# Performance work log

Hardware: AMD Instinct MI355X
Metric: run time of the kernel (lower is better)

## Reference

```python
import jax, jax.numpy as jnp
import numpy as np

D_MODEL = 2048
NUM_HEADS = 16
HEAD_DIM = D_MODEL // NUM_HEADS
SCALE = 1.0 / np.sqrt(HEAD_DIM).astype(np.float32)
NEG_INF = -1e9


def setup_inputs() -> dict:
    key = jax.random.key(0)
    ks = jax.random.split(key, 10)
    B, S = 2, 2048
    x = jax.random.normal(ks[0], (B, S, D_MODEL), dtype=jnp.float32)
    # causal lower-triangular mask, broadcastable over (B, H)
    causal_mask = jnp.tril(jnp.ones((S, S), dtype=jnp.int32))[None, None]
    init = 1.0 / np.sqrt(D_MODEL)
    def lin(kw, kb):
        W = jax.random.uniform(kw, (D_MODEL, D_MODEL), jnp.float32, -init, init)
        b = jax.random.uniform(kb, (D_MODEL,), jnp.float32, -init, init)
        return W, b
    Wq, bq = lin(ks[1], ks[2])
    Wk, bk = lin(ks[3], ks[4])
    Wv, bv = lin(ks[5], ks[6])
    Wo, bo = lin(ks[7], ks[8])
    return {"x": x, "causal_mask": causal_mask,
            "Wq": Wq, "bq": bq, "Wk": Wk, "bk": bk,
            "Wv": Wv, "bv": bv, "Wo": Wo, "bo": bo}


def reference(x, causal_mask, Wq, bq, Wk, bk, Wv, bv, Wo, bo):
    B, S, _ = x.shape
    def proj(W, b):
        # torch Linear: x @ W.T + b -> (B, H, S, Dh)
        y = jnp.einsum('bsd,ed->bse', x, W) + b
        return y.reshape(B, S, NUM_HEADS, HEAD_DIM).transpose(0, 2, 1, 3)
    q = proj(Wq, bq)
    k = proj(Wk, bk)
    v = proj(Wv, bv)
    # apply_rope is a no-op stub in the source; q, k unchanged.
    scores = jnp.einsum('bhqd,bhkd->bhqk', q, k) * SCALE
    scores = jnp.where(causal_mask == 0, NEG_INF, scores)
    attn = jax.nn.softmax(scores, axis=-1)
    out = jnp.einsum('bhqk,bhkd->bhqd', attn, v)
    out = out.transpose(0, 2, 1, 3).reshape(B, S, D_MODEL)
    return jnp.einsum('bsd,ed->bse', out, Wo) + bo
```

## Files before the change

kernel.cpp:

```cpp
#include <hip/hip_runtime.h>
#include <hip/hip_bf16.h>
#include <stdint.h>
#include <stddef.h>

typedef __bf16 bf16_t;
typedef __bf16 bf16x4_t __attribute__((ext_vector_type(4)));
typedef __bf16 bf16x8_t __attribute__((ext_vector_type(8)));
typedef float f32x4 __attribute__((ext_vector_type(4)));

#define D_MODEL 2048
#define NHEADS 16
#define HDIM 128
#define SEQ 2048
#define BATCH 2
#define MTOT (BATCH * SEQ)
#define SCALE_F 0.08838834764831845f
#define LOG2E 1.4426950408889634f
#define QSCALE (SCALE_F * LOG2E)
#define KT 64
#define NEGI -3.0e38f
#define MINIT -1.0e30f
#define DEFER_THR 8.0f

#define AS1 __attribute__((address_space(1)))
#define AS3 __attribute__((address_space(3)))

__device__ __forceinline__ void load_lds16(const bf16_t* g, bf16_t* l) {
  __builtin_amdgcn_global_load_lds((AS1 void*)(g), (AS3 void*)(l), 16, 0, 0);
}

__global__ void cast_kernel(const float* __restrict__ src, bf16_t* __restrict__ dst, int n4) {
  int i = blockIdx.x * blockDim.x + threadIdx.x;
  if (i < n4) {
    float4 v = ((const float4*)src)[i];
    bf16x4_t o;
    o.x = (bf16_t)v.x; o.y = (bf16_t)v.y; o.z = (bf16_t)v.z; o.w = (bf16_t)v.w;
    ((bf16x4_t*)dst)[i] = o;
  }
}

__global__ void cast4_kernel(const float* __restrict__ s0, const float* __restrict__ s1,
                             const float* __restrict__ s2, const float* __restrict__ s3,
                             bf16_t* __restrict__ dst, int n4) {
  int i = blockIdx.x * blockDim.x + threadIdx.x;
  int y = blockIdx.y;
  if (i < n4) {
    const float* src = (y == 0) ? s0 : (y == 1) ? s1 : (y == 2) ? s2 : s3;
    float4 v = ((const float4*)src)[i];
    bf16x4_t o;
    o.x = (bf16_t)v.x; o.y = (bf16_t)v.y; o.z = (bf16_t)v.z; o.w = (bf16_t)v.w;
    ((bf16x4_t*)(dst + (size_t)y * D_MODEL * D_MODEL / 4 * 4))[i] = o;
  }
}

__global__ __launch_bounds__(256) void gemm_fused(
    const bf16_t* __restrict__ A, const bf16_t* __restrict__ Bm, int mode,
    const float* __restrict__ bias0, const float* __restrict__ bias1,
    const float* __restrict__ bias2,
    bf16_t* __restrict__ Qo, bf16_t* __restrict__ Ko, bf16_t* __restrict__ Vto,
    float* __restrict__ Out) {
  const int K = 2048;
  __shared__ __align__(16) bf16_t lA[128 * 64];
  __shared__ __align__(16) bf16_t lB[128 * 64];
  const int m0 = blockIdx.x * 128;
  const int n0 = blockIdx.y * 128;
  const int t = threadIdx.x;
  const int w = t >> 6, lane = t & 63;
  const int wm = w & 1, wn = w >> 1;
  const int la = lane & 15, lb = lane >> 4;

  f32x4 acc[4][4];
  f32x4 zero = {0.f, 0.f, 0.f, 0.f};
#pragma unroll
  for (int i = 0; i < 4; i++)
#pragma unroll
    for (int j = 0; j < 4; j++) acc[i][j] = zero;

  const int row0 = t >> 3, cc = t & 7;
  const int ccs = cc ^ (row0 & 7);
  const bf16_t* gA = A + (size_t)(m0 + row0) * K + ccs * 8;
  const bf16_t* gB = Bm + (size_t)(n0 + row0) * K + ccs * 8;
  bf16_t* sA = lA + t * 8;
  bf16_t* sB = lB + t * 8;

  for (int k0 = 0; k0 < K; k0 += 64) {
    __syncthreads();
#pragma unroll
    for (int i = 0; i < 4; i++)
      load_lds16(gA + k0 + (size_t)(32 * i) * K, sA + 2048 * i);
#pragma unroll
    for (int i = 0; i < 4; i++)
      load_lds16(gB + k0 + (size_t)(32 * i) * K, sB + 2048 * i);
    __syncthreads();
#pragma unroll
    for (int ks = 0; ks < 2; ks++) {
      bf16x8_t af[4], bfr[4];
#pragma unroll
      for (int mt = 0; mt < 4; mt++) {
        int row = wm * 64 + mt * 16 + la;
        af[mt] = *(const bf16x8_t*)(lA + row * 64 + (((ks * 4 + lb) ^ (la & 7)) * 8));
      }
#pragma unroll
      for (int nt = 0; nt < 4; nt++) {
        int row = wn * 64 + nt * 16 + la;
        bfr[nt] = *(const bf16x8_t*)(lB + row * 64 + (((ks * 4 + lb) ^ (la & 7)) * 8));
      }
#pragma unroll
      for (int mt = 0; mt < 4; mt++)
#pragma unroll
        for (int nt = 0; nt < 4; nt++)
          acc[mt][nt] = __builtin_amdgcn_mfma_f32_16x16x32_bf16(af[mt], bfr[nt], acc[mt][nt], 0, 0, 0);
    }
  }

  if (mode == 0) {
#pragma unroll
    for (int mt = 0; mt < 4; mt++) {
#pragma unroll
      for (int nt = 0; nt < 4; nt++) {
        int m = m0 + wm * 64 + mt * 16 + lb * 4;
        int n = n0 + wn * 64 + nt * 16 + la;
        int b = m >> 11, s = m & 2047;
        int which = n >> 11, hd = n & 2047;
        int h = hd >> 7, d = hd & 127;
        float bv = (which == 0 ? bias0 : which == 1 ? bias1 : bias2)[hd];
        f32x4 v = acc[mt][nt];
        if (which == 2) {
          bf16_t* dst = Vto + ((size_t)(b * NHEADS + h) * HDIM + d) * SEQ + s;
          bf16x4_t pk;
          pk.x = (bf16_t)(v.x + bv); pk.y = (bf16_t)(v.y + bv);
          pk.z = (bf16_t)(v.z + bv); pk.w = (bf16_t)(v.w + bv);
          *(bf16x4_t*)dst = pk;
        } else {
          float sc = (which == 0) ? QSCALE : 1.0f;
          bf16_t* dst = (which == 0 ? Qo : Ko) + ((size_t)(b * NHEADS + h) * SEQ + s) * HDIM + d;
          dst[0]        = (bf16_t)((v.x + bv) * sc);
          dst[HDIM]     = (bf16_t)((v.y + bv) * sc);
          dst[2 * HDIM] = (bf16_t)((v.z + bv) * sc);
          dst[3 * HDIM] = (bf16_t)((v.w + bv) * sc);
        }
      }
    }
  } else {
#pragma unroll
    for (int mt = 0; mt < 4; mt++) {
#pragma unroll
      for (int nt = 0; nt < 4; nt++) {
        int m = m0 + wm * 64 + mt * 16 + lb * 4;
        int n = n0 + wn * 64 + nt * 16 + la;
        float bv = bias0[n];
        f32x4 v = acc[mt][nt];
        float* dst = Out + (size_t)m * D_MODEL + n;
        dst[0]           = v.x + bv;
        dst[D_MODEL]     = v.y + bv;
        dst[2 * D_MODEL] = v.z + bv;
        dst[3 * D_MODEL] = v.w + bv;
      }
    }
  }
}

__global__ __launch_bounds__(256, 2) void flash_attn(
    const bf16_t* __restrict__ Q, const bf16_t* __restrict__ Kg,
    const bf16_t* __restrict__ Vt, bf16_t* __restrict__ O,
    bf16_t* __restrict__ PO, float* __restrict__ ML) {
  __shared__ __align__(16) bf16_t lK[2][KT * 128];
  __shared__ __align__(16) bf16_t lV[128 * KT];
  __shared__ __align__(16) bf16_t lP[128 * 72];
  const int g = blockIdx.x;
  const int bh = g & 31, idx = g >> 5;
  const int t = threadIdx.x;
  const int w = t >> 6, lane = t & 63;
  const int la = lane & 15, lb = lane >> 4;
  const int qloc = w * 32 + la;

  const bf16_t* Qb = Q + (size_t)bh * SEQ * HDIM;
  const bf16_t* Kb = Kg + (size_t)bh * SEQ * HDIM;
  const bf16_t* Vb = Vt + (size_t)bh * HDIM * SEQ;
  const int b = bh >> 4, h = bh & 15;

  int nph, qts[2], k0s[2], k1s[2], slots[2];
  bool parts[2];
  if (idx < 8) {
    nph = 1; qts[0] = 8 + idx; k0s[0] = 0; k1s[0] = 17;
    parts[0] = true; slots[0] = (idx * 32 + bh) * 2;
  } else {
    int qtA = idx - 8;
    nph = 2;
    qts[0] = qtA; k0s[0] = 0; k1s[0] = 2 * qtA + 2; parts[0] = false; slots[0] = 0;
    qts[1] = 15 - qtA; k0s[1] = 17; k1s[1] = 32 - 2 * qtA;
    parts[1] = true; slots[1] = ((7 - qtA) * 32 + bh) * 2 + 1;
  }

  const int krow = t >> 4, kcc = t & 15;
  const int kccx = kcc ^ krow;
  const int vrow = t >> 3, vjc = t & 7;
  const int vccx = vjc ^ (vrow & 7);

  for (int ph = 0; ph < nph; ph++) {
    const int qt = qts[ph], kt0 = k0s[ph], kt1 = k1s[ph];
    const int q0 = qt * 128;

    bf16x8_t qf[2][4];
#pragma unroll
    for (int mt = 0; mt < 2; mt++)
#pragma unroll
      for (int ks = 0; ks < 4; ks++)
        qf[mt][ks] = *(const bf16x8_t*)(Qb + (size_t)(q0 + qloc + mt * 16) * HDIM + ks * 32 + lb * 8);

    f32x4 oacc[2][8];
    float mr[2] = {MINIT, MINIT}, lr[2] = {0.f, 0.f};
    f32x4 zero = {0.f, 0.f, 0.f, 0.f};
#pragma unroll
    for (int mt = 0; mt < 2; mt++)
#pragma unroll
      for (int dt = 0; dt < 8; dt++) oacc[mt][dt] = zero;

    {
      const int j0 = kt0 * KT;
#pragma unroll
      for (int i = 0; i < 4; i++)
        load_lds16(Kb + (size_t)(j0 + krow + 16 * i) * HDIM + kccx * 8,
                   lK[kt0 & 1] + (t + 256 * i) * 8);
    }

    for (int kt = kt0; kt < kt1; kt++) {
      const int j0 = kt * KT;
      const int cur = kt & 1;
      const bool pre = (kt + 1 < kt1);

      __syncthreads();

#pragma unroll
      for (int i = 0; i < 4; i++)
        load_lds16(Vb + (size_t)(vrow + 32 * i) * SEQ + j0 + vccx * 8,
                   lV + (t + 256 * i) * 8);
      if (pre) {
        const int jn = (kt + 1) * KT;
#pragma unroll
        for (int i = 0; i < 4; i++)
          load_lds16(Kb + (size_t)(jn + krow + 16 * i) * HDIM + kccx * 8,
                     lK[cur ^ 1] + (t + 256 * i) * 8);
      }

      f32x4 st[4][2];
#pragma unroll
      for (int nt = 0; nt < 4; nt++)
#pragma unroll
        for (int mt = 0; mt < 2; mt++) st[nt][mt] = zero;
#pragma unroll
      for (int ks = 0; ks < 4; ks++) {
#pragma unroll
        for (int nt = 0; nt < 4; nt++) {
          int j = nt * 16 + la;
          int ck = (ks * 4 + lb) ^ la;
          bf16x8_t kf = *(const bf16x8_t*)(lK[cur] + j * 128 + ck * 8);
#pragma unroll
          for (int mt = 0; mt < 2; mt++)
            st[nt][mt] = __builtin_amdgcn_mfma_f32_16x16x32_bf16(kf, qf[mt][ks], st[nt][mt], 0, 0, 0);
        }
      }

      const bool dm = (j0 + KT > q0);
#pragma unroll
      for (int mt = 0; mt < 2; mt++) {
        int qg = q0 + qloc + mt * 16;
        if (dm) {
#pragma unroll
          for (int nt = 0; nt < 4; nt++)
#pragma unroll
            for (int r = 0; r < 4; r++)
              if (j0 + nt * 16 + lb * 4 + r > qg) st[nt][mt][r] = NEGI;
        }
        float tm = NEGI;
#pragma unroll
        for (int nt = 0; nt < 4; nt++)
#pragma unroll
          for (int r = 0; r < 4; r++) tm = fmaxf(tm, st[nt][mt][r]);
        tm = fmaxf(tm, __shfl_xor(tm, 16));
        tm = fmaxf(tm, __shfl_xor(tm, 32));
        if (!__all(tm - mr[mt] <= DEFER_THR)) {
          float mnew = fmaxf(mr[mt], tm);
          float alpha = exp2f(mr[mt] - mnew);
          lr[mt] *= alpha;
#pragma unroll
          for (int dt = 0; dt < 8; dt++) oacc[mt][dt] *= alpha;
          mr[mt] = mnew;
        }
        float s = 0.f;
#pragma unroll
        for (int nt = 0; nt < 4; nt++) {
          f32x4 p;
#pragma unroll
          for (int r = 0; r < 4; r++) {
            p[r] = exp2f(st[nt][mt][r] - mr[mt]);
            s += p[r];
          }
          bf16x4_t pk;
          pk.x = (bf16_t)p[0]; pk.y = (bf16_t)p[1]; pk.z = (bf16_t)p[2]; pk.w = (bf16_t)p[3];
          *(bf16x4_t*)(lP + (qloc + mt * 16) * 72 + nt * 16 + lb * 4) = pk;
        }
        s += __shfl_xor(s, 16);
        s += __shfl_xor(s, 32);
        lr[mt] += s;
      }

      if (pre) {
        asm volatile("s_waitcnt vmcnt(4)" ::: "memory");
      } else {
        asm volatile("s_waitcnt vmcnt(0)" ::: "memory");
      }
      __builtin_amdgcn_s_barrier();

      bf16x8_t pf[2][2];
#pragma unroll
      for (int mt = 0; mt < 2; mt++)
#pragma unroll
        for (int ksv = 0; ksv < 2; ksv++)
          pf[mt][ksv] = *(const bf16x8_t*)(lP + (w * 32 + mt * 16 + la) * 72 + ksv * 32 + lb * 8);
#pragma unroll
      for (int dt = 0; dt < 8; dt++) {
        int d = dt * 16 + la;
#pragma unroll
        for (int ksv = 0; ksv < 2; ksv++) {
          int jc = (ksv * 4 + lb) ^ (d & 7);
          bf16x8_t vf = *(const bf16x8_t*)(lV + d * 64 + jc * 8);
#pragma unroll
          for (int mt = 0; mt < 2; mt++)
            oacc[mt][dt] = __builtin_amdgcn_mfma_f32_16x16x32_bf16(vf, pf[mt][ksv], oacc[mt][dt], 0, 0, 0);
        }
      }
    }

    if (!parts[ph]) {
#pragma unroll
      for (int mt = 0; mt < 2; mt++) {
        float inv = 1.0f / lr[mt];
        int q = q0 + qloc + mt * 16;
        bf16_t* dst = O + ((size_t)b * SEQ + q) * D_MODEL + h * HDIM + lb * 4;
#pragma unroll
        for (int dt = 0; dt < 8; dt++) {
          f32x4 v = oacc[mt][dt];
          bf16x4_t pk;
          pk.x = (bf16_t)(v[0] * inv); pk.y = (bf16_t)(v[1] * inv);
          pk.z = (bf16_t)(v[2] * inv); pk.w = (bf16_t)(v[3] * inv);
          *(bf16x4_t*)(dst + dt * 16) = pk;
        }
      }
    } else {
      const int slot = slots[ph];
      bf16_t* pob = PO + (size_t)slot * 128 * 128;
#pragma unroll
      for (int mt = 0; mt < 2; mt++) {
        int q = qloc + mt * 16;
        bf16_t* dst = pob + (size_t)q * 128 + lb * 4;
#pragma unroll
        for (int dt = 0; dt < 8; dt++) {
          f32x4 v = oacc[mt][dt];
          bf16x4_t pk;
          pk.x = (bf16_t)v[0]; pk.y = (bf16_t)v[1];
          pk.z = (bf16_t)v[2]; pk.w = (bf16_t)v[3];
          *(bf16x4_t*)(dst + dt * 16) = pk;
        }
        if (lb == 0) {
          float2 ml = make_float2(mr[mt], lr[mt]);
          *(float2*)(ML + ((size_t)slot * 128 + q) * 2) = ml;
        }
      }
    }
  }
}

__global__ void merge_kernel(const bf16_t* __restrict__ PO, const float* __restrict__ ML,
                             bf16_t* __restrict__ O) {
  const int qti = blockIdx.x >> 5, bh = blockIdx.x & 31;
  const int qt = 8 + qti;
  const int t = threadIdx.x;
  const int q = t >> 1, dh = (t & 1) * 64;
  const size_t s1 = ((size_t)(qti * 32 + bh)) * 2;
  const float* ml1 = ML + (s1 * 128 + q) * 2;
  const float* ml2 = ML + ((s1 + 1) * 128 + q) * 2;
  float m1 = ml1[0], l1 = ml1[1], m2 = ml2[0], l2 = ml2[1];
  float m = fmaxf(m1, m2);
  float w1 = exp2f(m1 - m), w2 = exp2f(m2 - m);
  float inv = 1.0f / (w1 * l1 + w2 * l2);
  w1 *= inv; w2 *= inv;
  const bf16_t* p1 = PO + (s1 * 128 + q) * 128 + dh;
  const bf16_t* p2 = PO + ((s1 + 1) * 128 + q) * 128 + dh;
  const int b = bh >> 4, h = bh & 15;
  bf16_t* dst = O + ((size_t)b * SEQ + qt * 128 + q) * D_MODEL + h * HDIM + dh;
#pragma unroll
  for (int i = 0; i < 8; i++) {
    bf16x8_t a = ((const bf16x8_t*)p1)[i];
    bf16x8_t c = ((const bf16x8_t*)p2)[i];
    bf16x8_t o;
#pragma unroll
    for (int e = 0; e < 8; e++)
      o[e] = (bf16_t)(w1 * (float)a[e] + w2 * (float)c[e]);
    ((bf16x8_t*)dst)[i] = o;
  }
}

extern "C" void kernel_launch(void* const* d_in, const int* in_sizes, int n_in,
                              void* d_out, int out_size, void* d_ws, size_t ws_size,
                              hipStream_t stream) {
  (void)in_sizes; (void)n_in; (void)out_size; (void)ws_size;
  const float* x  = (const float*)d_in[0];
  const float* Wq = (const float*)d_in[2];
  const float* bq = (const float*)d_in[3];
  const float* Wk = (const float*)d_in[4];
  const float* bk = (const float*)d_in[5];
  const float* Wv = (const float*)d_in[6];
  const float* bv = (const float*)d_in[7];
  const float* Wo = (const float*)d_in[8];
  const float* bo = (const float*)d_in[9];
  float* out = (float*)d_out;

  const size_t NBF = (size_t)MTOT * D_MODEL * sizeof(bf16_t);
  const size_t WBF = (size_t)D_MODEL * D_MODEL * sizeof(bf16_t);
  char* p = (char*)d_ws;
  bf16_t* xb   = (bf16_t*)p; p += NBF;
  bf16_t* Wcat = (bf16_t*)p; p += 4 * WBF;
  bf16_t* Qb   = (bf16_t*)p; p += NBF;
  bf16_t* Kb   = (bf16_t*)p; p += NBF;
  bf16_t* Vtb  = (bf16_t*)p; p += NBF;
  bf16_t* Wob  = Wcat + (size_t)3 * D_MODEL * D_MODEL;
  bf16_t* Ob   = xb;
  bf16_t* PO = Wcat;
  float*  ML = (float*)(Wcat + (size_t)512 * 128 * 128);

  const int WN4 = D_MODEL * D_MODEL / 4;
  const int XN4 = MTOT * D_MODEL / 4;
  cast_kernel<<<XN4 / 256, 256, 0, stream>>>(x, xb, XN4);
  cast4_kernel<<<dim3(WN4 / 256, 4), 256, 0, stream>>>(Wq, Wk, Wv, Wo, Wcat, WN4);

  gemm_fused<<<dim3(MTOT / 128, 6144 / 128), 256, 0, stream>>>(
      xb, Wcat, 0, bq, bk, bv, Qb, Kb, Vtb, nullptr);

  flash_attn<<<dim3(512), 256, 0, stream>>>(Qb, Kb, Vtb, Ob, PO, ML);
  merge_kernel<<<dim3(256), 256, 0, stream>>>(PO, ML, Ob);

  gemm_fused<<<dim3(MTOT / 128, D_MODEL / 128), 256, 0, stream>>>(
      Ob, Wob, 1, bo, nullptr, nullptr, nullptr, nullptr, nullptr, out);
}
```

Measured before the change: 375.2 us.

## Enlarge flash-attention query tile to 256 rows with double-buffered K/V staging

The attention kernel now runs 512 threads per block over 256-query tiles, which halves the grid and doubles the reuse of each K/V tile staged in shared memory. V is now double-buffered alongside K, and the next K/V tile is prefetched together. The mid-iteration vmcnt wait and barrier before the PV step are removed. The causal work-split schedule and the merge kernel are rescaled to match. In exchange, shared memory per block grows, occupancy may drop, and the grid of 256 blocks may leave some CUs underused.

```diff
diff --git a/kernel.cpp b/kernel.cpp
--- a/kernel.cpp
+++ b/kernel.cpp
@@ -160,13 +160,13 @@
   }
 }
 
-__global__ __launch_bounds__(256, 2) void flash_attn(
+__global__ __launch_bounds__(512, 2) void flash_attn(
     const bf16_t* __restrict__ Q, const bf16_t* __restrict__ Kg,
     const bf16_t* __restrict__ Vt, bf16_t* __restrict__ O,
     bf16_t* __restrict__ PO, float* __restrict__ ML) {
   __shared__ __align__(16) bf16_t lK[2][KT * 128];
-  __shared__ __align__(16) bf16_t lV[128 * KT];
-  __shared__ __align__(16) bf16_t lP[128 * 72];
+  __shared__ __align__(16) bf16_t lV[2][128 * KT];
+  __shared__ __align__(16) bf16_t lP[256 * 72];
   const int g = blockIdx.x;
   const int bh = g & 31, idx = g >> 5;
   const int t = threadIdx.x;
@@ -181,25 +181,36 @@
 
   int nph, qts[2], k0s[2], k1s[2], slots[2];
   bool parts[2];
-  if (idx < 8) {
-    nph = 1; qts[0] = 8 + idx; k0s[0] = 0; k1s[0] = 17;
+  if (idx < 4) {
+    nph = 1; qts[0] = 4 + idx; k0s[0] = 0; k1s[0] = 18;
     parts[0] = true; slots[0] = (idx * 32 + bh) * 2;
   } else {
-    int qtA = idx - 8;
+    int qtA = idx - 4;
     nph = 2;
-    qts[0] = qtA; k0s[0] = 0; k1s[0] = 2 * qtA + 2; parts[0] = false; slots[0] = 0;
-    qts[1] = 15 - qtA; k0s[1] = 17; k1s[1] = 32 - 2 * qtA;
-    parts[1] = true; slots[1] = ((7 - qtA) * 32 + bh) * 2 + 1;
+    qts[0] = qtA; k0s[0] = 0; k1s[0] = 4 * qtA + 4; parts[0] = false; slots[0] = 0;
+    qts[1] = 7 - qtA; k0s[1] = 18; k1s[1] = 32 - 4 * qtA;
+    parts[1] = true; slots[1] = ((3 - qtA) * 32 + bh) * 2 + 1;
   }
 
   const int krow = t >> 4, kcc = t & 15;
-  const int kccx = kcc ^ krow;
+  const int kccx = kcc ^ (krow & 15);
   const int vrow = t >> 3, vjc = t & 7;
   const int vccx = vjc ^ (vrow & 7);
 
+  auto stageKV = [&](int buf, int j0) {
+#pragma unroll
+    for (int i = 0; i < 2; i++)
+      load_lds16(Kb + (size_t)(j0 + krow + 32 * i) * HDIM + kccx * 8,
+                 lK[buf] + (t + 512 * i) * 8);
+#pragma unroll
+    for (int i = 0; i < 2; i++)
+      load_lds16(Vb + (size_t)(vrow + 64 * i) * SEQ + j0 + vccx * 8,
+                 lV[buf] + (t + 512 * i) * 8);
+  };
+
   for (int ph = 0; ph < nph; ph++) {
     const int qt = qts[ph], kt0 = k0s[ph], kt1 = k1s[ph];
-    const int q0 = qt * 128;
+    const int q0 = qt * 256;
 
     bf16x8_t qf[2][4];
 #pragma unroll
@@ -216,32 +227,15 @@
 #pragma unroll
       for (int dt = 0; dt < 8; dt++) oacc[mt][dt] = zero;
 
-    {
-      const int j0 = kt0 * KT;
-#pragma unroll
-      for (int i = 0; i < 4; i++)
-        load_lds16(Kb + (size_t)(j0 + krow + 16 * i) * HDIM + kccx * 8,
-                   lK[kt0 & 1] + (t + 256 * i) * 8);
-    }
+    __syncthreads();
+    stageKV(kt0 & 1, kt0 * KT);
 
     for (int kt = kt0; kt < kt1; kt++) {
       const int j0 = kt * KT;
       const int cur = kt & 1;
-      const bool pre = (kt + 1 < kt1);
 
       __syncthreads();
-
-#pragma unroll
-      for (int i = 0; i < 4; i++)
-        load_lds16(Vb + (size_t)(vrow + 32 * i) * SEQ + j0 + vccx * 8,
-                   lV + (t + 256 * i) * 8);
-      if (pre) {
-        const int jn = (kt + 1) * KT;
-#pragma unroll
-        for (int i = 0; i < 4; i++)
-          load_lds16(Kb + (size_t)(jn + krow + 16 * i) * HDIM + kccx * 8,
-                     lK[cur ^ 1] + (t + 256 * i) * 8);
-      }
+      if (kt + 1 < kt1) stageKV(cur ^ 1, (kt + 1) * KT);
 
       f32x4 st[4][2];
 #pragma unroll
@@ -305,26 +299,19 @@
         lr[mt] += s;
       }
 
-      if (pre) {
-        asm volatile("s_waitcnt vmcnt(4)" ::: "memory");
-      } else {
-        asm volatile("s_waitcnt vmcnt(0)" ::: "memory");
-      }
-      __builtin_amdgcn_s_barrier();
-
       bf16x8_t pf[2][2];
 #pragma unroll
       for (int mt = 0; mt < 2; mt++)
 #pragma unroll
         for (int ksv = 0; ksv < 2; ksv++)
-          pf[mt][ksv] = *(const bf16x8_t*)(lP + (w * 32 + mt * 16 + la) * 72 + ksv * 32 + lb * 8);
+          pf[mt][ksv] = *(const bf16x8_t*)(lP + (qloc + mt * 16) * 72 + ksv * 32 + lb * 8);
 #pragma unroll
       for (int dt = 0; dt < 8; dt++) {
         int d = dt * 16 + la;
 #pragma unroll
         for (int ksv = 0; ksv < 2; ksv++) {
           int jc = (ksv * 4 + lb) ^ (d & 7);
-          bf16x8_t vf = *(const bf16x8_t*)(lV + d * 64 + jc * 8);
+          bf16x8_t vf = *(const bf16x8_t*)(lV[cur] + d * 64 + jc * 8);
 #pragma unroll
           for (int mt = 0; mt < 2; mt++)
             oacc[mt][dt] = __builtin_amdgcn_mfma_f32_16x16x32_bf16(vf, pf[mt][ksv], oacc[mt][dt], 0, 0, 0);
@@ -349,7 +336,7 @@
       }
     } else {
       const int slot = slots[ph];
-      bf16_t* pob = PO + (size_t)slot * 128 * 128;
+      bf16_t* pob = PO + (size_t)slot * 256 * 128;
 #pragma unroll
       for (int mt = 0; mt < 2; mt++) {
         int q = qloc + mt * 16;
@@ -364,7 +351,7 @@
         }
         if (lb == 0) {
           float2 ml = make_float2(mr[mt], lr[mt]);
-          *(float2*)(ML + ((size_t)slot * 128 + q) * 2) = ml;
+          *(float2*)(ML + ((size_t)slot * 256 + q) * 2) = ml;
         }
       }
     }
@@ -374,21 +361,21 @@
 __global__ void merge_kernel(const bf16_t* __restrict__ PO, const float* __restrict__ ML,
                              bf16_t* __restrict__ O) {
   const int qti = blockIdx.x >> 5, bh = blockIdx.x & 31;
-  const int qt = 8 + qti;
+  const int qt = 4 + qti;
   const int t = threadIdx.x;
   const int q = t >> 1, dh = (t & 1) * 64;
   const size_t s1 = ((size_t)(qti * 32 + bh)) * 2;
-  const float* ml1 = ML + (s1 * 128 + q) * 2;
-  const float* ml2 = ML + ((s1 + 1) * 128 + q) * 2;
+  const float* ml1 = ML + (s1 * 256 + q) * 2;
+  const float* ml2 = ML + ((s1 + 1) * 256 + q) * 2;
   float m1 = ml1[0], l1 = ml1[1], m2 = ml2[0], l2 = ml2[1];
   float m = fmaxf(m1, m2);
   float w1 = exp2f(m1 - m), w2 = exp2f(m2 - m);
   float inv = 1.0f / (w1 * l1 + w2 * l2);
   w1 *= inv; w2 *= inv;
-  const bf16_t* p1 = PO + (s1 * 128 + q) * 128 + dh;
-  const bf16_t* p2 = PO + ((s1 + 1) * 128 + q) * 128 + dh;
+  const bf16_t* p1 = PO + (s1 * 256 + q) * 128 + dh;
+  const bf16_t* p2 = PO + ((s1 + 1) * 256 + q) * 128 + dh;
   const int b = bh >> 4, h = bh & 15;
-  bf16_t* dst = O + ((size_t)b * SEQ + qt * 128 + q) * D_MODEL + h * HDIM + dh;
+  bf16_t* dst = O + ((size_t)b * SEQ + qt * 256 + q) * D_MODEL + h * HDIM + dh;
 #pragma unroll
   for (int i = 0; i < 8; i++) {
     bf16x8_t a = ((const bf16x8_t*)p1)[i];
@@ -427,7 +414,7 @@
   bf16_t* Wob  = Wcat + (size_t)3 * D_MODEL * D_MODEL;
   bf16_t* Ob   = xb;
   bf16_t* PO = Wcat;
-  float*  ML = (float*)(Wcat + (size_t)512 * 128 * 128);
+  float*  ML = (float*)(Wcat + (size_t)256 * 256 * 128);
 
   const int WN4 = D_MODEL * D_MODEL / 4;
   const int XN4 = MTOT * D_MODEL / 4;
@@ -437,8 +424,8 @@
   gemm_fused<<<dim3(MTOT / 128, 6144 / 128), 256, 0, stream>>>(
       xb, Wcat, 0, bq, bk, bv, Qb, Kb, Vtb, nullptr);
 
-  flash_attn<<<dim3(512), 256, 0, stream>>>(Qb, Kb, Vtb, Ob, PO, ML);
-  merge_kernel<<<dim3(256), 256, 0, stream>>>(PO, ML, Ob);
+  flash_attn<<<dim3(256), 512, 0, stream>>>(Qb, Kb, Vtb, Ob, PO, ML);
+  merge_kernel<<<dim3(128), 512, 0, stream>>>(PO, ML, Ob);
 
   gemm_fused<<<dim3(MTOT / 128, D_MODEL / 128), 256, 0, stream>>>(
       Ob, Wob, 1, bo, nullptr, nullptr, nullptr, nullptr, nullptr, out);
```

Result: slower. 390.6 us (+4.1%).

## Double-buffer V with K in flash attention and drop the mid-loop barrier

Applied to the files above, without the earlier changes.

V tiles get their own double buffer and are prefetched one KV tile ahead together with K through a shared staging helper. Previously V was loaded synchronously in the current iteration. The explicit vmcnt wait and block barrier between softmax and the PV matmul are removed, since each warp only reads back its own P rows. The P scratch tile drops its 72-element padding in favour of an XOR swizzle. This raises LDS use to about 80KB per block, which could limit occupancy under the two-blocks launch bound.

```diff
diff --git a/kernel.cpp b/kernel.cpp
--- a/kernel.cpp
+++ b/kernel.cpp
@@ -165,8 +165,8 @@
     const bf16_t* __restrict__ Vt, bf16_t* __restrict__ O,
     bf16_t* __restrict__ PO, float* __restrict__ ML) {
   __shared__ __align__(16) bf16_t lK[2][KT * 128];
-  __shared__ __align__(16) bf16_t lV[128 * KT];
-  __shared__ __align__(16) bf16_t lP[128 * 72];
+  __shared__ __align__(16) bf16_t lV[2][128 * KT];
+  __shared__ __align__(16) bf16_t lP[128 * 64];
   const int g = blockIdx.x;
   const int bh = g & 31, idx = g >> 5;
   const int t = threadIdx.x;
@@ -197,6 +197,17 @@
   const int vrow = t >> 3, vjc = t & 7;
   const int vccx = vjc ^ (vrow & 7);
 
+  auto stageKV = [&](int buf, int j0) {
+#pragma unroll
+    for (int i = 0; i < 4; i++)
+      load_lds16(Kb + (size_t)(j0 + krow + 16 * i) * HDIM + kccx * 8,
+                 lK[buf] + (t + 256 * i) * 8);
+#pragma unroll
+    for (int i = 0; i < 4; i++)
+      load_lds16(Vb + (size_t)(vrow + 32 * i) * SEQ + j0 + vccx * 8,
+                 lV[buf] + (t + 256 * i) * 8);
+  };
+
   for (int ph = 0; ph < nph; ph++) {
     const int qt = qts[ph], kt0 = k0s[ph], kt1 = k1s[ph];
     const int q0 = qt * 128;
@@ -216,32 +227,15 @@
 #pragma unroll
       for (int dt = 0; dt < 8; dt++) oacc[mt][dt] = zero;
 
-    {
-      const int j0 = kt0 * KT;
-#pragma unroll
-      for (int i = 0; i < 4; i++)
-        load_lds16(Kb + (size_t)(j0 + krow + 16 * i) * HDIM + kccx * 8,
-                   lK[kt0 & 1] + (t + 256 * i) * 8);
-    }
+    __syncthreads();
+    stageKV(kt0 & 1, kt0 * KT);
 
     for (int kt = kt0; kt < kt1; kt++) {
       const int j0 = kt * KT;
       const int cur = kt & 1;
-      const bool pre = (kt + 1 < kt1);
 
       __syncthreads();
-
-#pragma unroll
-      for (int i = 0; i < 4; i++)
-        load_lds16(Vb + (size_t)(vrow + 32 * i) * SEQ + j0 + vccx * 8,
-                   lV + (t + 256 * i) * 8);
-      if (pre) {
-        const int jn = (kt + 1) * KT;
-#pragma unroll
-        for (int i = 0; i < 4; i++)
-          load_lds16(Kb + (size_t)(jn + krow + 16 * i) * HDIM + kccx * 8,
-                     lK[cur ^ 1] + (t + 256 * i) * 8);
-      }
+      if (kt + 1 < kt1) stageKV(cur ^ 1, (kt + 1) * KT);
 
       f32x4 st[4][2];
 #pragma unroll
@@ -298,33 +292,28 @@
           }
           bf16x4_t pk;
           pk.x = (bf16_t)p[0]; pk.y = (bf16_t)p[1]; pk.z = (bf16_t)p[2]; pk.w = (bf16_t)p[3];
-          *(bf16x4_t*)(lP + (qloc + mt * 16) * 72 + nt * 16 + lb * 4) = pk;
+          *(bf16x4_t*)(lP + (qloc + mt * 16) * 64 +
+                       (((nt * 4 + lb) ^ ((la & 7) << 1)) * 4)) = pk;
         }
         s += __shfl_xor(s, 16);
         s += __shfl_xor(s, 32);
         lr[mt] += s;
       }
 
-      if (pre) {
-        asm volatile("s_waitcnt vmcnt(4)" ::: "memory");
-      } else {
-        asm volatile("s_waitcnt vmcnt(0)" ::: "memory");
-      }
-      __builtin_amdgcn_s_barrier();
-
       bf16x8_t pf[2][2];
 #pragma unroll
       for (int mt = 0; mt < 2; mt++)
 #pragma unroll
         for (int ksv = 0; ksv < 2; ksv++)
-          pf[mt][ksv] = *(const bf16x8_t*)(lP + (w * 32 + mt * 16 + la) * 72 + ksv * 32 + lb * 8);
+          pf[mt][ksv] = *(const bf16x8_t*)(lP + (qloc + mt * 16) * 64 +
+                                           ((ksv * 32 + lb * 8) ^ ((la & 7) << 3)));
 #pragma unroll
       for (int dt = 0; dt < 8; dt++) {
         int d = dt * 16 + la;
 #pragma unroll
         for (int ksv = 0; ksv < 2; ksv++) {
           int jc = (ksv * 4 + lb) ^ (d & 7);
-          bf16x8_t vf = *(const bf16x8_t*)(lV + d * 64 + jc * 8);
+          bf16x8_t vf = *(const bf16x8_t*)(lV[cur] + d * 64 + jc * 8);
 #pragma unroll
           for (int mt = 0; mt < 2; mt++)
             oacc[mt][dt] = __builtin_amdgcn_mfma_f32_16x16x32_bf16(vf, pf[mt][ksv], oacc[mt][dt], 0, 0, 0);
```

New measurement: 383.3 us. +2.1%, slower.
